# Kernel tuning notes

Measured on AMD Instinct MI355X. Metric: run time of the kernel, lower is better.

## Reference

```python
import jax, jax.numpy as jnp
import numpy as np
import math

D = 768
H = 8
DK = D // H
FF = 1024
EPS = 1e-5


def _layer_norm(x, g, b):
    m = jnp.mean(x, axis=-1, keepdims=True)
    v = jnp.mean((x - m) ** 2, axis=-1, keepdims=True)
    return (x - m) * jax.lax.rsqrt(v + EPS) * g + b


def _mha(x, attention_mask, Wq, bq, Wv, bv, g, b):
    # x: (B,S,D); attention_mask: (B,S,1) bool (True = masked/padding query row)
    B, S, _ = x.shape
    q = (x @ Wq + bq).reshape(B, S, H, DK).transpose(0, 2, 1, 3)  # (B,H,S,dk)
    # NOTE: original code uses the V projection for BOTH k and v (k = self.V(x))
    kv = (x @ Wv + bv).reshape(B, S, H, DK).transpose(0, 2, 1, 3)
    k = kv
    v = kv
    w = jnp.einsum('bhqd,bhkd->bhqk', q, k) / math.sqrt(DK)  # (B,H,S,S)
    pad = attention_mask[:, None, :, :]                      # (B,1,S,1) -> bcast (B,1,S,S)
    causal = jnp.triu(jnp.ones((S, S), dtype=bool), k=1)     # look-ahead mask
    mask = pad | causal
    w = jnp.where(mask, jnp.float32(-1e9), w)
    # NOTE: original uses nn.Softmax(dim=2) -> softmax over the QUERY axis
    score = jax.nn.softmax(w, axis=2)
    o = jnp.einsum('bhqk,bhkd->bhqd', score, v)              # (B,H,S,dk)
    o = o.transpose(0, 2, 1, 3).reshape(B, S, D)
    return _layer_norm(o + x, g, b)


def _ffn(x, W1, b1, W2, b2, g, b):
    h = jax.nn.relu(x @ W1 + b1)
    return _layer_norm(h @ W2 + b2 + x, g, b)


def setup_inputs() -> dict:
    key = jax.random.key(0)
    ks = jax.random.split(key, 16)
    B, S = 8, 1024
    sc = 0.02
    inp = {
        'x': jax.random.normal(ks[0], (B, S, D), dtype=jnp.float32),
        'attention_mask': jax.random.randint(ks[1], (B, S, 1), 0, 2).astype(bool),
    }
    for i, pre in enumerate(['a1', 'a2']):
        inp[pre + '_Wq'] = jax.random.normal(ks[2 + 4 * i], (D, D), dtype=jnp.float32) * sc
        inp[pre + '_bq'] = jnp.zeros((D,), dtype=jnp.float32)
        inp[pre + '_Wv'] = jax.random.normal(ks[3 + 4 * i], (D, D), dtype=jnp.float32) * sc
        inp[pre + '_bv'] = jnp.zeros((D,), dtype=jnp.float32)
        inp[pre + '_g'] = jnp.ones((D,), dtype=jnp.float32)
        inp[pre + '_b'] = jnp.zeros((D,), dtype=jnp.float32)
    inp['f_W1'] = jax.random.normal(ks[10], (D, FF), dtype=jnp.float32) * sc
    inp['f_b1'] = jnp.zeros((FF,), dtype=jnp.float32)
    inp['f_W2'] = jax.random.normal(ks[11], (FF, D), dtype=jnp.float32) * sc
    inp['f_b2'] = jnp.zeros((D,), dtype=jnp.float32)
    inp['f_g'] = jnp.ones((D,), dtype=jnp.float32)
    inp['f_b'] = jnp.zeros((D,), dtype=jnp.float32)
    return inp


def reference(x, attention_mask,
              a1_Wq, a1_bq, a1_Wv, a1_bv, a1_g, a1_b,
              a2_Wq, a2_bq, a2_Wv, a2_bv, a2_g, a2_b,
              f_W1, f_b1, f_W2, f_b2, f_g, f_b):
    x = _mha(x, attention_mask, a1_Wq, a1_bq, a1_Wv, a1_bv, a1_g, a1_b)
    x = _mha(x, attention_mask, a2_Wq, a2_bq, a2_Wv, a2_bv, a2_g, a2_b)
    x = _ffn(x, f_W1, f_b1, f_W2, f_b2, f_g, f_b)
    return x
```

## Files before the change

### kernel.cpp

```cpp
#include <hip/hip_runtime.h>
#include <cstddef>

#define BB 8
#define SS 1024
#define DD 768
#define HH 8
#define DKK 96
#define FFF 1024
#define MM (BB*SS)
#define QVW 1536
#define SM_SCALE 0.10206207261596577f
#define NT2 8

typedef unsigned short ushort_t;
typedef short short8 __attribute__((ext_vector_type(8)));
typedef float f32x4 __attribute__((ext_vector_type(4)));
typedef ushort_t us4 __attribute__((ext_vector_type(4)));

__device__ __forceinline__ ushort_t f2b(float f) {
    union { float f; unsigned u; } x; x.f = f;
    unsigned r = x.u + 0x7fffu + ((x.u >> 16) & 1u);
    return (ushort_t)(r >> 16);
}
__device__ __forceinline__ float b2f(ushort_t u) {
    union { unsigned u; float f; } x; x.u = ((unsigned)u) << 16;
    return x.f;
}
__device__ __forceinline__ void gload16(const ushort_t* g, void* lds_base) {
    __builtin_amdgcn_global_load_lds(
        (const __attribute__((address_space(1))) unsigned int*)g,
        (__attribute__((address_space(3))) unsigned int*)lds_base, 16, 0, 0);
}

__global__ __launch_bounds__(256) void castWT(
    const float* __restrict__ W, ushort_t* __restrict__ Wt, int K, int N)
{
    __shared__ float T[32][33];
    const int tx = threadIdx.x & 31, ty = threadIdx.x >> 5;
    const int n0 = blockIdx.x * 32, k0 = blockIdx.y * 32;
    #pragma unroll
    for (int r = 0; r < 4; ++r)
        T[ty + 8*r][tx] = W[(size_t)(k0 + ty + 8*r) * N + n0 + tx];
    __syncthreads();
    #pragma unroll
    for (int r = 0; r < 4; ++r)
        Wt[(size_t)(n0 + ty + 8*r) * K + k0 + tx] = f2b(T[tx][ty + 8*r]);
}

__global__ __launch_bounds__(256) void castWT4(
    const float* __restrict__ Wa, const float* __restrict__ Wb,
    const float* __restrict__ Wc, const float* __restrict__ Wd,
    ushort_t* __restrict__ Ta, ushort_t* __restrict__ Tb,
    ushort_t* __restrict__ Tc, ushort_t* __restrict__ Td)
{
    __shared__ float T[32][33];
    const float* W; ushort_t* Wt;
    switch (blockIdx.z) {
        case 0:  W = Wa; Wt = Ta; break;
        case 1:  W = Wb; Wt = Tb; break;
        case 2:  W = Wc; Wt = Tc; break;
        default: W = Wd; Wt = Td; break;
    }
    const int tx = threadIdx.x & 31, ty = threadIdx.x >> 5;
    const int n0 = blockIdx.x * 32, k0 = blockIdx.y * 32;
    #pragma unroll
    for (int r = 0; r < 4; ++r)
        T[ty + 8*r][tx] = W[(size_t)(k0 + ty + 8*r) * DD + n0 + tx];
    __syncthreads();
    #pragma unroll
    for (int r = 0; r < 4; ++r)
        Wt[(size_t)(n0 + ty + 8*r) * DD + k0 + tx] = f2b(T[tx][ty + 8*r]);
}

__global__ __launch_bounds__(256) void cast_f2b(
    const float* __restrict__ in, ushort_t* __restrict__ out, int n4)
{
    const int i = blockIdx.x * 256 + threadIdx.x;
    if (i >= n4) return;
    const float4 v = ((const float4*)in)[i];
    us4 o; o.x = f2b(v.x); o.y = f2b(v.y); o.z = f2b(v.z); o.w = f2b(v.w);
    ((us4*)out)[i] = o;
}

template<int RELU>
__global__ __launch_bounds__(256) void gemm_bt(
    const ushort_t* __restrict__ A, const ushort_t* __restrict__ Bt,
    const float* __restrict__ bias, const float* __restrict__ bias2, int bN,
    ushort_t* __restrict__ C, int K, int N)
{
    __shared__ ushort_t S[128*136];
    ushort_t* As = S;
    ushort_t* Bs = S + 128*64;
    const int tid  = threadIdx.x;
    const int lane = tid & 63, wave = tid >> 6;
    const int wm = wave >> 1, wn = wave & 1;
    const int n = lane & 15, quad = lane >> 4;
    const int sx = n & 7;
    const int bm = blockIdx.y * 128, bn = blockIdx.x * 128;

    f32x4 acc[4][4];
    #pragma unroll
    for (int i = 0; i < 4; ++i)
        #pragma unroll
        for (int j = 0; j < 4; ++j) acc[i][j] = (f32x4){0.f, 0.f, 0.f, 0.f};

    for (int k0 = 0; k0 < K; k0 += 64) {
        #pragma unroll
        for (int it = 0; it < 4; ++it) {
            const int u   = (it*4 + wave)*64 + lane;
            const int row = u >> 3;
            const int c   = (u & 7) ^ (row & 7);
            gload16(A  + (size_t)(bm + row) * K + k0 + c*8, (char*)As + (it*4 + wave)*1024);
            gload16(Bt + (size_t)(bn + row) * K + k0 + c*8, (char*)Bs + (it*4 + wave)*1024);
        }
        __syncthreads();
        #pragma unroll
        for (int ks = 0; ks < 2; ++ks) {
            short8 af[4], bf[4];
            #pragma unroll
            for (int i = 0; i < 4; ++i)
                af[i] = *(short8*)&As[((wm*64 + i*16 + n)*8 + ((ks*4 + quad) ^ sx))*8];
            #pragma unroll
            for (int j = 0; j < 4; ++j)
                bf[j] = *(short8*)&Bs[((wn*64 + j*16 + n)*8 + ((ks*4 + quad) ^ sx))*8];
            #pragma unroll
            for (int i = 0; i < 4; ++i)
                #pragma unroll
                for (int j = 0; j < 4; ++j)
                    acc[i][j] = __builtin_amdgcn_mfma_f32_16x16x32_bf16(af[i], bf[j], acc[i][j], 0, 0, 0);
        }
        __syncthreads();
    }
    #pragma unroll
    for (int j = 0; j < 4; ++j) {
        const int col = wn*64 + j*16 + n;
        const int gcol = bn + col;
        const float bsv = (gcol < bN) ? bias[gcol] : bias2[gcol - bN];
        #pragma unroll
        for (int i = 0; i < 4; ++i) {
            const int lrow = wm*64 + i*16 + quad*4;
            #pragma unroll
            for (int r = 0; r < 4; ++r) {
                float v = acc[i][j][r] + bsv;
                if (RELU) v = fmaxf(v, 0.f);
                S[(lrow + r)*136 + col] = f2b(v);
            }
        }
    }
    __syncthreads();
    #pragma unroll
    for (int it = 0; it < 8; ++it) {
        const int u = it*256 + tid;
        const int grow = u >> 4, gc = u & 15;
        *(short8*)(C + (size_t)(bm + grow)*N + bn + gc*8) = *(short8*)&S[grow*136 + gc*8];
    }
}

__global__ __launch_bounds__(512, 4) void attn_sums(
    const ushort_t* __restrict__ QV, const int* __restrict__ amask,
    float* __restrict__ lpart)
{
    __shared__ ushort_t Ks[2][64*128];
    __shared__ float colsum[2][8][64];
    const int tid = threadIdx.x, lane = tid & 63, wave = tid >> 6;
    const int n = lane & 15, quad = lane >> 4, sx = n & 7;
    const int hwid = blockIdx.x;
    const int v = (hwid & 7) * 32 + (hwid >> 3);
    const int px = v & 3, h = (v >> 2) & 7, b = v >> 5;
    const ushort_t* Qh = QV + (size_t)b*SS*QVW + h*DKK;
    const ushort_t* Kh = QV + (size_t)b*SS*QVW + DD + h*DKK;
    float* lpq = lpart + (size_t)(b*HH + h)*NT2*SS;

    #pragma unroll
    for (int half = 0; half < 2; ++half) {
        const int qt2 = half ? (7 - px) : px;
        const int q0 = qt2 * 128;
        const int ktmax = 2*qt2 + 1;
        short8 aq[3];
        #pragma unroll
        for (int ks = 0; ks < 3; ++ks)
            aq[ks] = *(const short8*)(Qh + (size_t)(q0 + wave*16 + n)*QVW + ks*32 + quad*8);
        const int4 mv = *(const int4*)&amask[b*SS + q0 + wave*16 + quad*4];
        const int mr[4] = {mv.x, mv.y, mv.z, mv.w};
        #pragma unroll
        for (int it = 0; it < 2; ++it) {
            const int u = (it*8 + wave)*64 + lane;
            const int row = u >> 4, c = (u & 15) ^ (row & 7);
            if (c < 12)
                gload16(Kh + (size_t)row*QVW + c*8, (char*)Ks[0] + (it*8 + wave)*1024);
        }
        __syncthreads();

        int cur = 0;
        for (int kt = 0; kt <= ktmax; ++kt) {
            const int k0 = kt * 64;
            if (kt < ktmax) {
                #pragma unroll
                for (int it = 0; it < 2; ++it) {
                    const int u = (it*8 + wave)*64 + lane;
                    const int row = u >> 4, c = (u & 15) ^ (row & 7);
                    if (c < 12)
                        gload16(Kh + (size_t)(k0 + 64 + row)*QVW + c*8,
                                (char*)Ks[cur^1] + (it*8 + wave)*1024);
                }
            }
            if (kt > 0 && tid < 64) {
                const float s = colsum[cur^1][0][tid] + colsum[cur^1][1][tid]
                              + colsum[cur^1][2][tid] + colsum[cur^1][3][tid]
                              + colsum[cur^1][4][tid] + colsum[cur^1][5][tid]
                              + colsum[cur^1][6][tid] + colsum[cur^1][7][tid];
                lpq[(size_t)qt2*SS + (k0 - 64) + tid] = s;
            }
            #pragma unroll
            for (int ns = 0; ns < 4; ++ns) {
                f32x4 sa = (f32x4){0.f, 0.f, 0.f, 0.f};
                #pragma unroll
                for (int ks = 0; ks < 3; ++ks) {
                    const short8 bk = *(short8*)&Ks[cur][((ns*16 + n)*16 + ((ks*4 + quad) ^ sx))*8];
                    sa = __builtin_amdgcn_mfma_f32_16x16x32_bf16(aq[ks], bk, sa, 0, 0, 0);
                }
                const int kl = ns*16 + n;
                const int keyg = k0 + kl;
                float s = 0.f;
                #pragma unroll
                for (int r = 0; r < 4; ++r) {
                    const int qg = q0 + wave*16 + quad*4 + r;
                    const bool dead = (mr[r] != 0) || (keyg > qg);
                    s += dead ? 0.f : __expf(sa[r] * SM_SCALE);
                }
                s += __shfl_xor(s, 16);
                s += __shfl_xor(s, 32);
                if (quad == 0) colsum[cur][wave][kl] = s;
            }
            __syncthreads();
            cur ^= 1;
        }
        if (tid < 64) {
            const int pb = ktmax & 1;
            const float s = colsum[pb][0][tid] + colsum[pb][1][tid]
                          + colsum[pb][2][tid] + colsum[pb][3][tid]
                          + colsum[pb][4][tid] + colsum[pb][5][tid]
                          + colsum[pb][6][tid] + colsum[pb][7][tid];
            lpq[(size_t)qt2*SS + ktmax*64 + tid] = s;
        }
    }
}

__global__ __launch_bounds__(256) void transpose_scale(
    const ushort_t* __restrict__ QV, const float* __restrict__ lpart,
    ushort_t* __restrict__ Vt)
{
    __shared__ ushort_t T[64][104];
    __shared__ float rlv[64];
    const int tid = threadIdx.x;
    const int k0 = blockIdx.x * 64, h = blockIdx.y, b = blockIdx.z;
    const ushort_t* src = QV + (size_t)b*SS*QVW + DD + h*DKK;
    for (int s = tid; s < 768; s += 256) {
        const int r = s / 12, c = s % 12;
        *(short8*)&T[r][c*8] = *(const short8*)(src + (size_t)(k0 + r)*QVW + c*8);
    }
    if (tid < 64) {
        const float* lp = lpart + (size_t)(b*HH + h)*NT2*SS;
        float l = 0.f;
        for (int qt2 = k0 >> 7; qt2 < NT2; ++qt2) l += lp[(size_t)qt2*SS + k0 + tid];
        rlv[tid] = (l > 0.f) ? (1.f / l) : 0.f;
    }
    __syncthreads();
    ushort_t* dst = Vt + ((size_t)b*HH + h)*DKK*SS;
    for (int s = tid; s < 768; s += 256) {
        const int dk = s >> 3, c = s & 7;
        short8 v;
        #pragma unroll
        for (int i = 0; i < 8; ++i)
            v[i] = (short)f2b(b2f(T[c*8 + i][dk]) * rlv[c*8 + i]);
        *(short8*)(dst + (size_t)dk*SS + k0 + c*8) = v;
    }
}

__global__ __launch_bounds__(512, 4) void attn_pv_re(
    const ushort_t* __restrict__ QV, const int* __restrict__ amask,
    const ushort_t* __restrict__ Vt, ushort_t* __restrict__ O)
{
    __shared__ ushort_t Ks[2][64*128];
    __shared__ ushort_t Vs[2][96*64];
    __shared__ ushort_t Es[128*64];
    const int tid = threadIdx.x, lane = tid & 63, wave = tid >> 6;
    const int n = lane & 15, quad = lane >> 4, sx = n & 7;
    const int hwid = blockIdx.x;
    const int v = (hwid & 7) * 32 + (hwid >> 3);
    const int px = v & 3, h = (v >> 2) & 7, b = v >> 5;
    const ushort_t* Qh = QV + (size_t)b*SS*QVW + h*DKK;
    const ushort_t* Kh = QV + (size_t)b*SS*QVW + DD + h*DKK;
    const ushort_t* Vth = Vt + ((size_t)b*HH + h)*DKK*SS;

    #pragma unroll
    for (int half = 0; half < 2; ++half) {
        const int qt2 = half ? (7 - px) : px;
        const int q0 = qt2 * 128;
        const int ktmax = 2*qt2 + 1;
        short8 aq[3];
        #pragma unroll
        for (int ks = 0; ks < 3; ++ks)
            aq[ks] = *(const short8*)(Qh + (size_t)(q0 + wave*16 + n)*QVW + ks*32 + quad*8);
        const int4 mv = *(const int4*)&amask[b*SS + q0 + wave*16 + quad*4];
        const int mr[4] = {mv.x, mv.y, mv.z, mv.w};
        #pragma unroll
        for (int it = 0; it < 2; ++it) {
            const int u = (it*8 + wave)*64 + lane;
            const int row = u >> 4, c = (u & 15) ^ (row & 7);
            if (c < 12)
                gload16(Kh + (size_t)row*QVW + c*8, (char*)Ks[0] + (it*8 + wave)*1024);
        }
        #pragma unroll
        for (int it = 0; it < 2; ++it) {
            if (it*8 + wave < 12) {
                const int u = (it*8 + wave)*64 + lane;
                const int row = u >> 3, c = (u & 7) ^ (row & 7);
                gload16(Vth + (size_t)row*SS + c*8, (char*)Vs[0] + (it*8 + wave)*1024);
            }
        }
        __syncthreads();

        f32x4 acc[6];
        #pragma unroll
        for (int t = 0; t < 6; ++t) acc[t] = (f32x4){0.f, 0.f, 0.f, 0.f};

        int cur = 0;
        for (int kt = 0; kt <= ktmax; ++kt) {
            const int k0 = kt * 64;
            if (kt < ktmax) {
                #pragma unroll
                for (int it = 0; it < 2; ++it) {
                    const int u = (it*8 + wave)*64 + lane;
                    const int row = u >> 4, c = (u & 15) ^ (row & 7);
                    if (c < 12)
                        gload16(Kh + (size_t)(k0 + 64 + row)*QVW + c*8,
                                (char*)Ks[cur^1] + (it*8 + wave)*1024);
                }
                #pragma unroll
                for (int it = 0; it < 2; ++it) {
                    if (it*8 + wave < 12) {
                        const int u = (it*8 + wave)*64 + lane;
                        const int row = u >> 3, c = (u & 7) ^ (row & 7);
                        gload16(Vth + (size_t)row*SS + k0 + 64 + c*8,
                                (char*)Vs[cur^1] + (it*8 + wave)*1024);
                    }
                }
            }
            #pragma unroll
            for (int ns = 0; ns < 4; ++ns) {
                f32x4 sa = (f32x4){0.f, 0.f, 0.f, 0.f};
                #pragma unroll
                for (int ks = 0; ks < 3; ++ks) {
                    const short8 bk = *(short8*)&Ks[cur][((ns*16 + n)*16 + ((ks*4 + quad) ^ sx))*8];
                    sa = __builtin_amdgcn_mfma_f32_16x16x32_bf16(aq[ks], bk, sa, 0, 0, 0);
                }
                const int kl = ns*16 + n;
                const int keyg = k0 + kl;
                #pragma unroll
                for (int r = 0; r < 4; ++r) {
                    const int lq = quad*4 + r;
                    const int trow = wave*16 + lq;
                    const bool dead = (mr[r] != 0) || (keyg > q0 + trow);
                    const float e = dead ? 0.f : __expf(sa[r] * SM_SCALE);
                    Es[trow*64 + (((kl >> 3) ^ (lq & 7)) * 8) + (kl & 7)] = f2b(e);
                }
            }
            asm volatile("s_waitcnt lgkmcnt(0)" ::: "memory");
            __builtin_amdgcn_sched_barrier(0);

            #pragma unroll
            for (int kk = 0; kk < 2; ++kk) {
                const short8 ae = *(short8*)&Es[((wave*16 + n)*8 + ((kk*4 + quad) ^ sx))*8];
                #pragma unroll
                for (int nt = 0; nt < 6; ++nt) {
                    const short8 bv = *(short8*)&Vs[cur][((nt*16 + n)*8 + ((kk*4 + quad) ^ sx))*8];
                    acc[nt] = __builtin_amdgcn_mfma_f32_16x16x32_bf16(ae, bv, acc[nt], 0, 0, 0);
                }
            }
            __syncthreads();
            cur ^= 1;
        }
        #pragma unroll
        for (int nt = 0; nt < 6; ++nt) {
            #pragma unroll
            for (int r = 0; r < 4; ++r) {
                const int q = q0 + wave*16 + quad*4 + r;
                O[((size_t)b*SS + q)*DD + h*DKK + nt*16 + n] = f2b(acc[nt][r]);
            }
        }
    }
}

__device__ __forceinline__ float block_sum256(float s, float* tmp4)
{
    #pragma unroll
    for (int off = 32; off > 0; off >>= 1) s += __shfl_down(s, off);
    __syncthreads();
    if ((threadIdx.x & 63) == 0) tmp4[threadIdx.x >> 6] = s;
    __syncthreads();
    return tmp4[0] + tmp4[1] + tmp4[2] + tmp4[3];
}

template<int XBF, int RBF, int OUTF32>
__global__ __launch_bounds__(256) void resid_ln(
    const void* __restrict__ X, const void* __restrict__ R,
    const float* __restrict__ g, const float* __restrict__ beta,
    ushort_t* __restrict__ OutB, float* __restrict__ OutF)
{
    __shared__ float tmp4[4];
    const int row = blockIdx.x;
    const int tid = threadIdx.x;
    float v[3], s = 0.f;
    #pragma unroll
    for (int i = 0; i < 3; ++i) {
        const size_t idx = (size_t)row * DD + tid + 256*i;
        const float xv = XBF ? b2f(((const ushort_t*)X)[idx]) : ((const float*)X)[idx];
        const float rv = RBF ? b2f(((const ushort_t*)R)[idx]) : ((const float*)R)[idx];
        v[i] = xv + rv;
        s += v[i];
    }
    const float mu = block_sum256(s, tmp4) * (1.f / DD);
    float qv = 0.f;
    #pragma unroll
    for (int i = 0; i < 3; ++i) { const float d = v[i] - mu; qv += d * d; }
    const float inv = rsqrtf(block_sum256(qv, tmp4) * (1.f / DD) + 1e-5f);
    #pragma unroll
    for (int i = 0; i < 3; ++i) {
        const int c = tid + 256*i;
        const float o = (v[i] - mu) * inv * g[c] + beta[c];
        if (OUTF32) OutF[(size_t)row * DD + c] = o;
        else        OutB[(size_t)row * DD + c] = f2b(o);
    }
}

extern "C" void kernel_launch(void* const* d_in, const int* in_sizes, int n_in,
                              void* d_out, int out_size, void* d_ws, size_t ws_size,
                              hipStream_t stream)
{
    (void)in_sizes; (void)n_in; (void)out_size; (void)ws_size;
    const float* x0    = (const float*)d_in[0];
    const int*   amask = (const int*)d_in[1];
    const float* a1_Wq = (const float*)d_in[2];
    const float* a1_bq = (const float*)d_in[3];
    const float* a1_Wv = (const float*)d_in[4];
    const float* a1_bv = (const float*)d_in[5];
    const float* a1_g  = (const float*)d_in[6];
    const float* a1_b  = (const float*)d_in[7];
    const float* a2_Wq = (const float*)d_in[8];
    const float* a2_bq = (const float*)d_in[9];
    const float* a2_Wv = (const float*)d_in[10];
    const float* a2_bv = (const float*)d_in[11];
    const float* a2_g  = (const float*)d_in[12];
    const float* a2_b  = (const float*)d_in[13];
    const float* f_W1  = (const float*)d_in[14];
    const float* f_b1  = (const float*)d_in[15];
    const float* f_W2  = (const float*)d_in[16];
    const float* f_b2  = (const float*)d_in[17];
    const float* f_g   = (const float*)d_in[18];
    const float* f_b   = (const float*)d_in[19];

    char* ws = (char*)d_ws;
    size_t off = 0;
    auto alloc = [&](size_t bytes) { void* p = ws + off; off += (bytes + 255) & ~(size_t)255; return p; };
    ushort_t* WqvT1 = (ushort_t*)alloc((size_t)QVW*DD*2);
    ushort_t* WqvT2 = (ushort_t*)alloc((size_t)QVW*DD*2);
    ushort_t* W1T   = (ushort_t*)alloc((size_t)DD*FFF*2);
    ushort_t* W2T   = (ushort_t*)alloc((size_t)DD*FFF*2);
    ushort_t* xb0   = (ushort_t*)alloc((size_t)MM*DD*2);
    ushort_t* xb1   = (ushort_t*)alloc((size_t)MM*DD*2);
    ushort_t* xb2   = (ushort_t*)alloc((size_t)MM*DD*2);
    ushort_t* Ob    = (ushort_t*)alloc((size_t)MM*DD*2);
    ushort_t* QVb   = (ushort_t*)alloc((size_t)MM*QVW*2);
    ushort_t* hb    = QVb;
    ushort_t* Vtb   = (ushort_t*)alloc((size_t)MM*DD*2);
    float* lpart = (float*)alloc((size_t)BB*HH*NT2*SS*4);
    float* out = (float*)d_out;

    const dim3 blk(256);
    const dim3 blk512(512);
    const dim3 gat(256);
    const dim3 gtr(SS/64, HH, BB);
    const dim3 gqv(QVW/128, MM/128);
    const dim3 gf1(FFF/128, MM/128);
    const dim3 gf2(DD/128, MM/128);

    castWT4<<<dim3(DD/32, DD/32, 4), blk, 0, stream>>>(
        a1_Wq, a1_Wv, a2_Wq, a2_Wv,
        WqvT1, WqvT1 + (size_t)DD*DD, WqvT2, WqvT2 + (size_t)DD*DD);
    castWT<<<dim3(FFF/32, DD/32), blk, 0, stream>>>(f_W1, W1T, DD, FFF);
    castWT<<<dim3(DD/32, FFF/32), blk, 0, stream>>>(f_W2, W2T, FFF, DD);
    cast_f2b<<<(MM*DD/4 + 255)/256, blk, 0, stream>>>(x0, xb0, MM*DD/4);

    gemm_bt<0><<<gqv, blk, 0, stream>>>(xb0, WqvT1, a1_bq, a1_bv, DD, QVb, DD, QVW);
    attn_sums<<<gat, blk512, 0, stream>>>(QVb, amask, lpart);
    transpose_scale<<<gtr, blk, 0, stream>>>(QVb, lpart, Vtb);
    attn_pv_re<<<gat, blk512, 0, stream>>>(QVb, amask, Vtb, Ob);
    resid_ln<1,0,0><<<dim3(MM), blk, 0, stream>>>(Ob, x0, a1_g, a1_b, xb1, nullptr);

    gemm_bt<0><<<gqv, blk, 0, stream>>>(xb1, WqvT2, a2_bq, a2_bv, DD, QVb, DD, QVW);
    attn_sums<<<gat, blk512, 0, stream>>>(QVb, amask, lpart);
    transpose_scale<<<gtr, blk, 0, stream>>>(QVb, lpart, Vtb);
    attn_pv_re<<<gat, blk512, 0, stream>>>(QVb, amask, Vtb, Ob);
    resid_ln<1,1,0><<<dim3(MM), blk, 0, stream>>>(Ob, xb1, a2_g, a2_b, xb2, nullptr);

    gemm_bt<1><<<gf1, blk, 0, stream>>>(xb2, W1T, f_b1, f_b1, FFF, hb, DD, FFF);
    gemm_bt<0><<<gf2, blk, 0, stream>>>(hb, W2T, f_b2, f_b2, DD, Ob, FFF, DD);
    resid_ln<1,1,1><<<dim3(MM), blk, 0, stream>>>(Ob, xb2, f_g, f_b, nullptr, out);
}
```

Measured before the change: 394.2 us.

## Load K/V straight from global into registers and drop block-wide syncs in attention

Measured after the change: 591.3 us. +50.0%, slower.

```diff
diff --git a/kernel.cpp b/kernel.cpp
--- a/kernel.cpp
+++ b/kernel.cpp
@@ -160,16 +160,14 @@
     const ushort_t* __restrict__ QV, const int* __restrict__ amask,
     float* __restrict__ lpart)
 {
-    __shared__ ushort_t Ks[2][64*128];
-    __shared__ float colsum[2][8][64];
     const int tid = threadIdx.x, lane = tid & 63, wave = tid >> 6;
-    const int n = lane & 15, quad = lane >> 4, sx = n & 7;
+    const int n = lane & 15, quad = lane >> 4;
     const int hwid = blockIdx.x;
     const int v = (hwid & 7) * 32 + (hwid >> 3);
     const int px = v & 3, h = (v >> 2) & 7, b = v >> 5;
     const ushort_t* Qh = QV + (size_t)b*SS*QVW + h*DKK;
     const ushort_t* Kh = QV + (size_t)b*SS*QVW + DD + h*DKK;
-    float* lpq = lpart + (size_t)(b*HH + h)*NT2*SS;
+    float* lpq = lpart + (size_t)(b*HH + h)*NT2*8*SS;
 
     #pragma unroll
     for (int half = 0; half < 2; ++half) {
@@ -182,41 +180,17 @@
             aq[ks] = *(const short8*)(Qh + (size_t)(q0 + wave*16 + n)*QVW + ks*32 + quad*8);
         const int4 mv = *(const int4*)&amask[b*SS + q0 + wave*16 + quad*4];
         const int mr[4] = {mv.x, mv.y, mv.z, mv.w};
-        #pragma unroll
-        for (int it = 0; it < 2; ++it) {
-            const int u = (it*8 + wave)*64 + lane;
-            const int row = u >> 4, c = (u & 15) ^ (row & 7);
-            if (c < 12)
-                gload16(Kh + (size_t)row*QVW + c*8, (char*)Ks[0] + (it*8 + wave)*1024);
-        }
-        __syncthreads();
-
-        int cur = 0;
+
+        float* lpw = lpq + ((size_t)qt2*8 + wave)*SS;
         for (int kt = 0; kt <= ktmax; ++kt) {
             const int k0 = kt * 64;
-            if (kt < ktmax) {
-                #pragma unroll
-                for (int it = 0; it < 2; ++it) {
-                    const int u = (it*8 + wave)*64 + lane;
-                    const int row = u >> 4, c = (u & 15) ^ (row & 7);
-                    if (c < 12)
-                        gload16(Kh + (size_t)(k0 + 64 + row)*QVW + c*8,
-                                (char*)Ks[cur^1] + (it*8 + wave)*1024);
-                }
-            }
-            if (kt > 0 && tid < 64) {
-                const float s = colsum[cur^1][0][tid] + colsum[cur^1][1][tid]
-                              + colsum[cur^1][2][tid] + colsum[cur^1][3][tid]
-                              + colsum[cur^1][4][tid] + colsum[cur^1][5][tid]
-                              + colsum[cur^1][6][tid] + colsum[cur^1][7][tid];
-                lpq[(size_t)qt2*SS + (k0 - 64) + tid] = s;
-            }
             #pragma unroll
             for (int ns = 0; ns < 4; ++ns) {
+                const ushort_t* kr = Kh + (size_t)(k0 + ns*16 + n)*QVW + quad*8;
                 f32x4 sa = (f32x4){0.f, 0.f, 0.f, 0.f};
                 #pragma unroll
                 for (int ks = 0; ks < 3; ++ks) {
-                    const short8 bk = *(short8*)&Ks[cur][((ns*16 + n)*16 + ((ks*4 + quad) ^ sx))*8];
+                    const short8 bk = *(const short8*)(kr + ks*32);
                     sa = __builtin_amdgcn_mfma_f32_16x16x32_bf16(aq[ks], bk, sa, 0, 0, 0);
                 }
                 const int kl = ns*16 + n;
@@ -230,18 +204,8 @@
                 }
                 s += __shfl_xor(s, 16);
                 s += __shfl_xor(s, 32);
-                if (quad == 0) colsum[cur][wave][kl] = s;
+                if (quad == 0) lpw[k0 + kl] = s;
             }
-            __syncthreads();
-            cur ^= 1;
-        }
-        if (tid < 64) {
-            const int pb = ktmax & 1;
-            const float s = colsum[pb][0][tid] + colsum[pb][1][tid]
-                          + colsum[pb][2][tid] + colsum[pb][3][tid]
-                          + colsum[pb][4][tid] + colsum[pb][5][tid]
-                          + colsum[pb][6][tid] + colsum[pb][7][tid];
-            lpq[(size_t)qt2*SS + ktmax*64 + tid] = s;
         }
     }
 }
@@ -251,6 +215,7 @@
     ushort_t* __restrict__ Vt)
 {
     __shared__ ushort_t T[64][104];
+    __shared__ float rpart[4][64];
     __shared__ float rlv[64];
     const int tid = threadIdx.x;
     const int k0 = blockIdx.x * 64, h = blockIdx.y, b = blockIdx.z;
@@ -259,10 +224,22 @@
         const int r = s / 12, c = s % 12;
         *(short8*)&T[r][c*8] = *(const short8*)(src + (size_t)(k0 + r)*QVW + c*8);
     }
+    {
+        const float* lp = lpart + (size_t)(b*HH + h)*NT2*8*SS;
+        const int part = tid >> 6, kk = tid & 63;
+        const int qtmin = k0 >> 7;
+        float l = 0.f;
+        #pragma unroll
+        for (int c = 0; c < 16; ++c) {
+            const int cc = part*16 + c;
+            const int qt2 = cc >> 3, w = cc & 7;
+            if (qt2 >= qtmin) l += lp[((size_t)qt2*8 + w)*SS + k0 + kk];
+        }
+        rpart[part][kk] = l;
+    }
+    __syncthreads();
     if (tid < 64) {
-        const float* lp = lpart + (size_t)(b*HH + h)*NT2*SS;
-        float l = 0.f;
-        for (int qt2 = k0 >> 7; qt2 < NT2; ++qt2) l += lp[(size_t)qt2*SS + k0 + tid];
+        const float l = rpart[0][tid] + rpart[1][tid] + rpart[2][tid] + rpart[3][tid];
         rlv[tid] = (l > 0.f) ? (1.f / l) : 0.f;
     }
     __syncthreads();
@@ -281,8 +258,6 @@
     const ushort_t* __restrict__ QV, const int* __restrict__ amask,
     const ushort_t* __restrict__ Vt, ushort_t* __restrict__ O)
 {
-    __shared__ ushort_t Ks[2][64*128];
-    __shared__ ushort_t Vs[2][96*64];
     __shared__ ushort_t Es[128*64];
     const int tid = threadIdx.x, lane = tid & 63, wave = tid >> 6;
     const int n = lane & 15, quad = lane >> 4, sx = n & 7;
@@ -304,55 +279,24 @@
             aq[ks] = *(const short8*)(Qh + (size_t)(q0 + wave*16 + n)*QVW + ks*32 + quad*8);
         const int4 mv = *(const int4*)&amask[b*SS + q0 + wave*16 + quad*4];
         const int mr[4] = {mv.x, mv.y, mv.z, mv.w};
-        #pragma unroll
-        for (int it = 0; it < 2; ++it) {
-            const int u = (it*8 + wave)*64 + lane;
-            const int row = u >> 4, c = (u & 15) ^ (row & 7);
-            if (c < 12)
-                gload16(Kh + (size_t)row*QVW + c*8, (char*)Ks[0] + (it*8 + wave)*1024);
-        }
-        #pragma unroll
-        for (int it = 0; it < 2; ++it) {
-            if (it*8 + wave < 12) {
-                const int u = (it*8 + wave)*64 + lane;
-                const int row = u >> 3, c = (u & 7) ^ (row & 7);
-                gload16(Vth + (size_t)row*SS + c*8, (char*)Vs[0] + (it*8 + wave)*1024);
-            }
-        }
-        __syncthreads();
 
         f32x4 acc[6];
         #pragma unroll
         for (int t = 0; t < 6; ++t) acc[t] = (f32x4){0.f, 0.f, 0.f, 0.f};
 
-        int cur = 0;
         for (int kt = 0; kt <= ktmax; ++kt) {
             const int k0 = kt * 64;
-            if (kt < ktmax) {
-                #pragma unroll
-                for (int it = 0; it < 2; ++it) {
-                    const int u = (it*8 + wave)*64 + lane;
-                    const int row = u >> 4, c = (u & 15) ^ (row & 7);
-                    if (c < 12)
-                        gload16(Kh + (size_t)(k0 + 64 + row)*QVW + c*8,
-                                (char*)Ks[cur^1] + (it*8 + wave)*1024);
-                }
-                #pragma unroll
-                for (int it = 0; it < 2; ++it) {
-                    if (it*8 + wave < 12) {
-                        const int u = (it*8 + wave)*64 + lane;
-                        const int row = u >> 3, c = (u & 7) ^ (row & 7);
-                        gload16(Vth + (size_t)row*SS + k0 + 64 + c*8,
-                                (char*)Vs[cur^1] + (it*8 + wave)*1024);
-                    }
-                }
-            }
+            short8 bv0[6];
+            #pragma unroll
+            for (int nt = 0; nt < 6; ++nt)
+                bv0[nt] = *(const short8*)(Vth + (size_t)(nt*16 + n)*SS + k0 + quad*8);
             #pragma unroll
             for (int ns = 0; ns < 4; ++ns) {
+                const ushort_t* kr = Kh + (size_t)(k0 + ns*16 + n)*QVW + quad*8;
                 f32x4 sa = (f32x4){0.f, 0.f, 0.f, 0.f};
                 #pragma unroll
                 for (int ks = 0; ks < 3; ++ks) {
-                    const short8 bk = *(short8*)&Ks[cur][((ns*16 + n)*16 + ((ks*4 + quad) ^ sx))*8];
+                    const short8 bk = *(const short8*)(kr + ks*32);
                     sa = __builtin_amdgcn_mfma_f32_16x16x32_bf16(aq[ks], bk, sa, 0, 0, 0);
                 }
                 const int kl = ns*16 + n;
@@ -366,20 +310,23 @@
                     Es[trow*64 + (((kl >> 3) ^ (lq & 7)) * 8) + (kl & 7)] = f2b(e);
                 }
             }
+            short8 bv1[6];
+            #pragma unroll
+            for (int nt = 0; nt < 6; ++nt)
+                bv1[nt] = *(const short8*)(Vth + (size_t)(nt*16 + n)*SS + k0 + 32 + quad*8);
             asm volatile("s_waitcnt lgkmcnt(0)" ::: "memory");
             __builtin_amdgcn_sched_barrier(0);
 
-            #pragma unroll
-            for (int kk = 0; kk < 2; ++kk) {
-                const short8 ae = *(short8*)&Es[((wave*16 + n)*8 + ((kk*4 + quad) ^ sx))*8];
-                #pragma unroll
-                for (int nt = 0; nt < 6; ++nt) {
-                    const short8 bv = *(short8*)&Vs[cur][((nt*16 + n)*8 + ((kk*4 + quad) ^ sx))*8];
-                    acc[nt] = __builtin_amdgcn_mfma_f32_16x16x32_bf16(ae, bv, acc[nt], 0, 0, 0);
-                }
+            {
+                const short8 ae0 = *(short8*)&Es[((wave*16 + n)*8 + (quad ^ sx))*8];
+                #pragma unroll
+                for (int nt = 0; nt < 6; ++nt)
+                    acc[nt] = __builtin_amdgcn_mfma_f32_16x16x32_bf16(ae0, bv0[nt], acc[nt], 0, 0, 0);
+                const short8 ae1 = *(short8*)&Es[((wave*16 + n)*8 + ((4 + quad) ^ sx))*8];
+                #pragma unroll
+                for (int nt = 0; nt < 6; ++nt)
+                    acc[nt] = __builtin_amdgcn_mfma_f32_16x16x32_bf16(ae1, bv1[nt], acc[nt], 0, 0, 0);
             }
-            __syncthreads();
-            cur ^= 1;
         }
         #pragma unroll
         for (int nt = 0; nt < 6; ++nt) {
@@ -474,7 +421,7 @@
     ushort_t* QVb   = (ushort_t*)alloc((size_t)MM*QVW*2);
     ushort_t* hb    = QVb;
     ushort_t* Vtb   = (ushort_t*)alloc((size_t)MM*DD*2);
-    float* lpart = (float*)alloc((size_t)BB*HH*NT2*SS*4);
+    float* lpart = (float*)alloc((size_t)BB*HH*NT2*8*SS*4);
     float* out = (float*)d_out;
 
     const dim3 blk(256);
```
